# Performance work log

Hardware: AMD Instinct MI355X
Metric: run time of the kernel (lower is better)

Reference implementation:

```python
import jax, jax.numpy as jnp
import numpy as np

B, N, NB, E, H, A, K, D = 32, 512, 10, 1024, 256, 82, 4, 3


def setup_inputs() -> dict:
    key = jax.random.key(0)
    ks = iter(jax.random.split(key, 64))
    f = lambda shape: jax.random.normal(next(ks), shape, jnp.float32) * 0.05
    inp = {
        "atom_fea": jax.random.normal(next(ks), (B, N, A), jnp.float32),
        "bond_fea": jax.random.normal(next(ks), (B, E, 6), jnp.float32),
        "d_anb": jax.random.randint(next(ks), (B, N, NB), 0, N),
        "d_bnb": jax.random.randint(next(ks), (B, N, NB), 0, E),
        "d_nbs_mask": (jax.random.uniform(next(ks), (B, N, NB)) < 0.8).astype(jnp.float32),
        "d_mask": (jax.random.uniform(next(ks), (B, N)) < 0.9).astype(jnp.float32),
        "Wv": f((A, H)), "bv": f((H,)),
        "Wa_main": f((D, K, H, H)), "ba_main": f((D, K, H)),
        "Wa_super": f((D, K, H, H)), "ba_super": f((D, K, H)),
        "Wm": f((D, K, H, H)), "bm": f((D, K, H)),
        "Wbmm": f((D, K, H)), "bbmm": f((D, K)),
        "Wm2s": f((D, K * H, H)), "bm2s": f((D, H)),
        "Ws2m": f((D, H, H)), "bs2m": f((D, H)),
        "Wsup": f((D, H, H)), "bsup": f((D, H)),
        "Wzm1": f((D, H, H)), "bzm1": f((D, H)),
        "Wzm2": f((D, H, H)), "bzm2": f((D, H)),
        "Wzs1": f((D, H, H)), "bzs1": f((D, H)),
        "Wzs2": f((D, H, H)), "bzs2": f((D, H)),
        "Wu2": f((D, H + 6, H)), "bu2": f((D, H)),
        "Wu1": f((D, 2 * H, H)), "bu1": f((D, H)),
    }
    return inp


def mask_softmax(a, mask):
    a_max = jnp.max(a, -1, keepdims=True)
    e = jnp.exp(a - a_max) * mask
    return e / (jnp.sum(e, -1, keepdims=True) + 1e-6)


def _forward(atom_fea, bond_fea, d_nbs_mask, d_mask,
             Wv, bv, Wa_main, ba_main, Wa_super, ba_super, Wm, bm, Wbmm, bbmm,
             Wm2s, bm2s, Ws2m, bs2m, Wsup, bsup,
             Wzm1, bzm1, Wzm2, bzm2, Wzs1, bzs1, Wzs2, bzs2,
             Wu2, bu2, Wu1, bu1, d_anb, d_bnb):
    Bn = atom_fea.shape[0]
    bidx = jnp.arange(Bn)[:, None, None]
    # vertex embedding (default leaky_relu slope 0.01)
    vf = jax.nn.leaky_relu(atom_fea @ Wv + bv, 0.01)            # [B,N,H]
    sf = jnp.sum(vf * d_mask[:, :, None], axis=1, keepdims=True)  # [B,1,H]
    mask3 = d_nbs_mask[..., None]                               # [B,N,NB,1]
    for d in range(D):
        # --- multi-head main->super attention (vectorized over heads k) ---
        a_main = jnp.tanh(jnp.einsum('bnh,khj->bknj', vf, Wa_main[d]) + ba_main[d][None, :, None, :])
        a_super = jnp.tanh(jnp.einsum('boh,khj->bkoj', sf, Wa_super[d]) + ba_super[d][None, :, None, :])
        a = jnp.einsum('bknh,kh->bkn', a_main * a_super, Wbmm[d]) + bbmm[d][None, :, None]
        attn = mask_softmax(a, d_mask[:, None, :])               # [B,K,N]
        mvf = jnp.einsum('bnh,khj->bknj', vf, Wm[d]) + bm[d][None, :, None, :]
        m2s = jnp.einsum('bkn,bknh->bkh', attn, mvf).reshape(Bn, 1, K * H)
        main_to_super = jnp.tanh(m2s @ Wm2s[d] + bm2s[d])        # [B,1,H]
        # --- wln unit: gather neighbors, MLP, masked sum (slope 0.1) ---
        vnei = vf[bidx, d_anb]                                   # [B,N,NB,H]
        enei = bond_fea[bidx, d_bnb]                             # [B,N,NB,6]
        lnei = jnp.concatenate([vnei, enei], -1)                 # [B,N,NB,H+6]
        nei = jax.nn.leaky_relu(lnei @ Wu2[d] + bu2[d], 0.1)
        nei = jnp.sum(nei * mask3, axis=2)                       # [B,N,H]
        main_self = jax.nn.leaky_relu(jnp.concatenate([vf, nei], -1) @ Wu1[d] + bu1[d], 0.1)
        # --- GRU-style gated updates ---
        super_to_main = jnp.tanh(sf @ Ws2m[d] + bs2m[d])         # [B,1,H]
        super_self = jnp.tanh(sf @ Wsup[d] + bsup[d])            # [B,1,H]
        z_main = jax.nn.sigmoid(main_self @ Wzm1[d] + bzm1[d] + super_to_main @ Wzm2[d] + bzm2[d])
        vf = (1 - z_main) * main_self + z_main * super_to_main
        z_sup = jax.nn.sigmoid(super_self @ Wzs1[d] + bzs1[d] + main_to_super @ Wzs2[d] + bzs2[d])
        sf = (1 - z_sup) * super_self + z_sup * main_to_super    # [B,1,H]; sum over dim 1 is a no-op
    return vf, sf


def reference(atom_fea, bond_fea, d_anb, d_bnb, d_nbs_mask, d_mask,
              Wv, bv, Wa_main, ba_main, Wa_super, ba_super, Wm, bm, Wbmm, bbmm,
              Wm2s, bm2s, Ws2m, bs2m, Wsup, bsup,
              Wzm1, bzm1, Wzm2, bzm2, Wzs1, bzs1, Wzs2, bzs2,
              Wu2, bu2, Wu1, bu1):
    return _forward(atom_fea, bond_fea, d_nbs_mask, d_mask,
                    Wv, bv, Wa_main, ba_main, Wa_super, ba_super, Wm, bm, Wbmm, bbmm,
                    Wm2s, bm2s, Ws2m, bs2m, Wsup, bsup,
                    Wzm1, bzm1, Wzm2, bzm2, Wzs1, bzs1, Wzs2, bzs2,
                    Wu2, bu2, Wu1, bu1, d_anb, d_bnb)
```

## Files before the change

kernel.cpp:

```cpp
#include <hip/hip_runtime.h>
#include <hip/hip_bf16.h>

#define B_ 32
#define N_ 512
#define NB_ 10
#define E_ 1024
#define H_ 256
#define A_ 82
#define K_ 4
#define D_ 3
#define M_ (B_*N_)

typedef unsigned short u16;
typedef __attribute__((ext_vector_type(8))) short bf16x8;
typedef __attribute__((ext_vector_type(4))) float f32x4;

__device__ __forceinline__ float b2f(u16 u){
    unsigned int x = ((unsigned int)u) << 16;
    return __builtin_bit_cast(float, x);
}
__device__ __forceinline__ u16 f2b(float f){
    unsigned int x = __builtin_bit_cast(unsigned int, f);
    unsigned int lsb = (x >> 16) & 1u;
    x += 0x7fffu + lsb;
    return (u16)(x >> 16);
}
__device__ __forceinline__ float sigmoidf_(float x){ return 1.f/(1.f+expf(-x)); }

static constexpr int CVT_N[31] = {
    B_*E_*6, B_*N_*NB_, B_*N_,
    A_*H_, H_,
    D_*K_*H_*H_, D_*K_*H_, D_*K_*H_*H_, D_*K_*H_,
    D_*K_*H_*H_, D_*K_*H_, D_*K_*H_, D_*K_,
    D_*K_*H_*H_, D_*H_, D_*H_*H_, D_*H_,
    D_*H_*H_, D_*H_, D_*H_*H_, D_*H_,
    D_*H_*H_, D_*H_, D_*H_*H_, D_*H_,
    D_*H_*H_, D_*H_, D_*(H_+6)*H_, D_*H_,
    D_*2*H_*H_, D_*H_
};
struct Offs { long v[32]; };
static constexpr Offs mk_offs(){
    Offs o{}; o.v[0]=0;
    for(int i=0;i<31;i++) o.v[i+1]=o.v[i]+CVT_N[i];
    return o;
}
static constexpr Offs CVT_OFF = mk_offs();

struct Ptrs { const void* p[31]; };

__global__ void k_detect(const unsigned short* __restrict__ wv_raw, int* __restrict__ flag){
    float v = b2f(wv_raw[threadIdx.x]);
    bool plaus = (v==v) && (fabsf(v) < 100.0f);
    unsigned long long m = __ballot(plaus);
    if (threadIdx.x==0) *flag = (m == ~0ULL) ? 1 : 0;
}

__global__ void k_cvt(Ptrs ptrs, float* __restrict__ dst, const int* __restrict__ flag){
    int t = blockIdx.y;
    int n = CVT_N[t];
    int i4 = blockIdx.x*256 + threadIdx.x;
    if (i4*4 >= n) return;
    const void* src = ptrs.p[t];
    float4 o;
    if (*flag){
        ushort4 u = ((const ushort4*)src)[i4];
        o.x=b2f(u.x); o.y=b2f(u.y); o.z=b2f(u.z); o.w=b2f(u.w);
    } else {
        o = ((const float4*)src)[i4];
    }
    *(float4*)(dst + CVT_OFF.v[t] + (size_t)i4*4) = o;
}

__global__ void k_wt(const float* __restrict__ Wam, const float* __restrict__ Wu2,
                     const float* __restrict__ Wu1, const float* __restrict__ Wzm1,
                     u16* __restrict__ WT){
    int mi = blockIdx.z;
    const float* src;
    if (mi<12)      src = Wam  + (size_t)mi*H_*H_;
    else if (mi<15) src = Wu2  + (size_t)(mi-12)*(H_+6)*H_;
    else if (mi<18) src = Wu1  + (size_t)(mi-15)*2*H_*H_;
    else if (mi<21) src = Wu1  + (size_t)(mi-18)*2*H_*H_ + (size_t)H_*H_;
    else            src = Wzm1 + (size_t)(mi-21)*H_*H_;
    __shared__ float t[32][33];
    int x = threadIdx.x, y = threadIdx.y;
    int k0 = blockIdx.y*32, n0 = blockIdx.x*32;
    for(int yy=y; yy<32; yy+=8) t[yy][x] = src[(size_t)(k0+yy)*H_ + n0+x];
    __syncthreads();
    u16* dst = WT + ((size_t)mi*8 + (k0>>5))*(256*32);
    for(int yy=y; yy<32; yy+=8) dst[(size_t)(n0+yy)*32 + x] = f2b(t[x][yy]);
}

__global__ void k_embed(const u16* __restrict__ atom, const float* __restrict__ Wv,
                        const float* __restrict__ bv, float* __restrict__ vf,
                        const int* __restrict__ flag){
    __shared__ float arow[8][A_];
    int r0 = blockIdx.x*8; int j = threadIdx.x;
    int fl = *flag;
    for(int i=j;i<8*A_;i+=256){
        int r=i/A_, a=i-r*A_;
        arow[r][a] = fl ? b2f(atom[(size_t)(r0+r)*A_+a])
                        : ((const float*)atom)[(size_t)(r0+r)*A_+a];
    }
    __syncthreads();
    float acc[8];
    float bj = bv[j];
    #pragma unroll
    for(int r=0;r<8;r++) acc[r]=bj;
    for(int a=0;a<A_;a++){
        float w = Wv[a*H_+j];
        #pragma unroll
        for(int r=0;r<8;r++) acc[r] += arow[r][a]*w;
    }
    #pragma unroll
    for(int r=0;r<8;r++){
        float v = acc[r];
        vf[(size_t)(r0+r)*H_+j] = v>0.f ? v : 0.01f*v;
    }
}

__global__ void k_sf0(const float* __restrict__ vf, const float* __restrict__ dmask,
                      float* __restrict__ sf){
    int b = blockIdx.x, h = threadIdx.x;
    __shared__ float mk[N_];
    for(int n=threadIdx.x;n<N_;n+=256) mk[n] = dmask[b*N_+n];
    __syncthreads();
    float s=0.f;
    #pragma unroll 8
    for(int n=0;n<N_;n++) s += mk[n]*vf[((size_t)b*N_+n)*H_ + h];
    sf[b*H_+h]=s;
}

__global__ void k_s1(int d, const float* __restrict__ sf,
    const float* __restrict__ Was, const float* __restrict__ bas,
    const float* __restrict__ Wbmm,
    const float* __restrict__ Ws2m, const float* __restrict__ bs2m,
    const float* __restrict__ Wsup, const float* __restrict__ bsup,
    float* __restrict__ asw, float* __restrict__ s2m, float* __restrict__ ssf)
{
    int b = blockIdx.x, m = blockIdx.y, j = threadIdx.x;
    __shared__ float sfl[H_];
    sfl[j] = sf[b*H_+j];
    __syncthreads();
    const float* W; float bias;
    if (m < 4){ W = Was + (size_t)(d*K_+m)*H_*H_; bias = bas[(d*K_+m)*H_+j]; }
    else if (m==4){ W = Ws2m + (size_t)d*H_*H_; bias = bs2m[d*H_+j]; }
    else { W = Wsup + (size_t)d*H_*H_; bias = bsup[d*H_+j]; }
    float acc = bias;
    #pragma unroll 8
    for(int h=0;h<H_;h++) acc += sfl[h]*W[h*H_+j];
    float v = tanhf(acc);
    if (m < 4) asw[(b*K_+m)*H_+j] = v * Wbmm[(d*K_+m)*H_+j];
    else if (m==4) s2m[b*H_+j] = v;
    else ssf[b*H_+j] = v;
}

__global__ void k_s2(int d, const float* __restrict__ s2m,
    const float* __restrict__ Wzm2, const float* __restrict__ bzm2,
    float* __restrict__ stm2p)
{
    int b=blockIdx.x, c=blockIdx.y, j=threadIdx.x;
    __shared__ float xl[64];
    if (j<64) xl[j] = s2m[b*H_ + c*64 + j];
    __syncthreads();
    const float* W = Wzm2 + (size_t)d*H_*H_ + (size_t)(c*64)*H_;
    float acc = (c==0) ? bzm2[d*H_+j] : 0.f;
    #pragma unroll 8
    for(int h=0;h<64;h++) acc += xl[h]*W[h*H_+j];
    stm2p[((size_t)c*B_+b)*H_+j] = acc;
}

__device__ __forceinline__ void mfma_core_wt(const float* __restrict__ A,
    const u16* __restrict__ WTg, f32x4 acc[2][8],
    u16* __restrict__ Als, u16* __restrict__ Ws)
{
    const int LSA = 40, LSW = 40;
    int tid = threadIdx.x;
    int lane = tid & 63, wave = tid >> 6;
    int wy = wave >> 1, wx = wave & 1;
    int quad = lane >> 4, l15 = lane & 15;
    #pragma unroll
    for(int mt=0;mt<2;mt++)
        #pragma unroll
        for(int nt=0;nt<8;nt++) acc[mt][nt] = (f32x4){0.f,0.f,0.f,0.f};
    int arow = tid >> 2;
    int ak8  = (tid & 3) * 8;
    for(int k0=0;k0<H_;k0+=32){
        float4 a0 = *(const float4*)(A + (size_t)arow*H_ + k0 + ak8);
        float4 a1 = *(const float4*)(A + (size_t)arow*H_ + k0 + ak8 + 4);
        union { u16 u[8]; bf16x8 v; } ua;
        ua.u[0]=f2b(a0.x); ua.u[1]=f2b(a0.y); ua.u[2]=f2b(a0.z); ua.u[3]=f2b(a0.w);
        ua.u[4]=f2b(a1.x); ua.u[5]=f2b(a1.y); ua.u[6]=f2b(a1.z); ua.u[7]=f2b(a1.w);
        *(bf16x8*)(Als + arow*LSA + ak8) = ua.v;
        const u16* wsrc = WTg + (size_t)(k0>>5)*(256*32) + tid*32;
        #pragma unroll
        for(int c=0;c<4;c++)
            *(bf16x8*)(Ws + tid*LSW + c*8) = *(const bf16x8*)(wsrc + c*8);
        __syncthreads();
        bf16x8 af[2], bfr[8];
        #pragma unroll
        for(int mt=0;mt<2;mt++)
            af[mt] = *(const bf16x8*)(Als + (wy*32+mt*16+l15)*LSA + quad*8);
        #pragma unroll
        for(int nt=0;nt<8;nt++)
            bfr[nt] = *(const bf16x8*)(Ws + (wx*128+nt*16+l15)*LSW + quad*8);
        #pragma unroll
        for(int mt=0;mt<2;mt++)
            #pragma unroll
            for(int nt=0;nt<8;nt++)
                acc[mt][nt] = __builtin_amdgcn_mfma_f32_16x16x32_bf16(
                    af[mt], bfr[nt], acc[mt][nt], 0,0,0);
        __syncthreads();
    }
}

__global__ __launch_bounds__(256) void k_gemm_big(int d, const float* __restrict__ vf,
    const u16* __restrict__ WT, const float* __restrict__ ba_main,
    const float* __restrict__ bbmm, const float* __restrict__ bu1,
    const float* __restrict__ asw, float* __restrict__ score,
    float* __restrict__ proj_u2, float* __restrict__ pu1a)
{
    __shared__ u16 Als[64*40];
    __shared__ u16 Ws[256*40];
    __shared__ float sred[64][33];
    int m0 = blockIdx.x*64;
    int seg = blockIdx.y;
    int b = m0 >> 9;
    int mi;
    if (seg < 4)      mi = d*4+seg;
    else if (seg==4)  mi = 12+d;
    else              mi = 15+d;
    f32x4 acc[2][8];
    mfma_core_wt(vf + (size_t)m0*H_, WT + (size_t)mi*H_*H_, acc, Als, Ws);
    int tid=threadIdx.x, lane=tid&63, wave=tid>>6;
    int wy=wave>>1, wx=wave&1, quad=lane>>4, l15=lane&15;
    if (seg < 4){
        const float* aswp = asw + (size_t)(b*K_+seg)*H_;
        const float* bap  = ba_main + (size_t)(d*K_+seg)*H_;
        float bbv[8], awv[8];
        #pragma unroll
        for(int nt=0;nt<8;nt++){
            int col = wx*128+nt*16+l15;
            bbv[nt]=bap[col]; awv[nt]=aswp[col];
        }
        #pragma unroll
        for(int mt=0;mt<2;mt++)
            #pragma unroll
            for(int r=0;r<4;r++){
                float p=0.f;
                #pragma unroll
                for(int nt=0;nt<8;nt++)
                    p += tanhf(acc[mt][nt][r]+bbv[nt])*awv[nt];
                int row = wy*32+mt*16+quad*4+r;
                sred[row][wx*16+l15] = p;
            }
        __syncthreads();
        if (tid < 64){
            float s=0.f;
            #pragma unroll 8
            for(int i=0;i<32;i++) s += sred[tid][i];
            score[(size_t)(b*K_+seg)*N_ + (m0&511) + tid] = s + bbmm[d*K_+seg];
        }
    } else if (seg==4){
        #pragma unroll
        for(int mt=0;mt<2;mt++)
            #pragma unroll
            for(int nt=0;nt<8;nt++){
                int col = wx*128+nt*16+l15;
                #pragma unroll
                for(int r=0;r<4;r++){
                    int row = m0 + wy*32+mt*16+quad*4+r;
                    proj_u2[(size_t)row*H_+col] = acc[mt][nt][r];
                }
            }
    } else {
        const float* bp = bu1 + d*H_;
        #pragma unroll
        for(int mt=0;mt<2;mt++)
            #pragma unroll
            for(int nt=0;nt<8;nt++){
                int col = wx*128+nt*16+l15;
                float bb = bp[col];
                #pragma unroll
                for(int r=0;r<4;r++){
                    int row = m0 + wy*32+mt*16+quad*4+r;
                    pu1a[(size_t)row*H_+col] = acc[mt][nt][r] + bb;
                }
            }
    }
}

__global__ __launch_bounds__(256) void k_mainself(int d, const float* __restrict__ nei,
    const u16* __restrict__ WT, float* __restrict__ pu)
{
    __shared__ u16 Als[64*40];
    __shared__ u16 Ws[256*40];
    int m0 = blockIdx.x*64;
    f32x4 acc[2][8];
    mfma_core_wt(nei + (size_t)m0*H_, WT + (size_t)(18+d)*H_*H_, acc, Als, Ws);
    int tid=threadIdx.x, lane=tid&63, wave=tid>>6;
    int wy=wave>>1, wx=wave&1, quad=lane>>4, l15=lane&15;
    #pragma unroll
    for(int mt=0;mt<2;mt++)
        #pragma unroll
        for(int nt=0;nt<8;nt++){
            int col = wx*128+nt*16+l15;
            #pragma unroll
            for(int r=0;r<4;r++){
                int row = m0 + wy*32+mt*16+quad*4+r;
                float v = acc[mt][nt][r] + pu[(size_t)row*H_+col];
                v = v>0.f? v : 0.1f*v;
                pu[(size_t)row*H_+col] = v;
            }
        }
}

__global__ __launch_bounds__(256) void k_update(int d, const float* __restrict__ main_self,
    const u16* __restrict__ WT, const float* __restrict__ bzm1,
    const float* __restrict__ stm2p, const float* __restrict__ s2m, float* __restrict__ vf)
{
    __shared__ u16 Als[64*40];
    __shared__ u16 Ws[256*40];
    int m0 = blockIdx.x*64; int b = m0>>9;
    f32x4 acc[2][8];
    mfma_core_wt(main_self + (size_t)m0*H_, WT + (size_t)(21+d)*H_*H_, acc, Als, Ws);
    int tid=threadIdx.x, lane=tid&63, wave=tid>>6;
    int wy=wave>>1, wx=wave&1, quad=lane>>4, l15=lane&15;
    #pragma unroll
    for(int mt=0;mt<2;mt++)
        #pragma unroll
        for(int nt=0;nt<8;nt++){
            int col = wx*128+nt*16+l15;
            float bz = bzm1[d*H_+col];
            float st = stm2p[(size_t)(0*B_+b)*H_+col] + stm2p[(size_t)(1*B_+b)*H_+col]
                     + stm2p[(size_t)(2*B_+b)*H_+col] + stm2p[(size_t)(3*B_+b)*H_+col];
            float sm = s2m[b*H_+col];
            #pragma unroll
            for(int r=0;r<4;r++){
                int row = m0 + wy*32+mt*16+quad*4+r;
                float z = sigmoidf_(acc[mt][nt][r] + bz + st);
                float ms = main_self[(size_t)row*H_+col];
                vf[(size_t)row*H_+col] = (1.f-z)*ms + z*sm;
            }
        }
}

__global__ void k_softmax(float* __restrict__ score, const float* __restrict__ dmask,
                          float* __restrict__ sumattn){
    int b = blockIdx.x, k = blockIdx.y;
    int tid = threadIdx.x;
    __shared__ float sh[256];
    float* a = score + (size_t)(b*K_+k)*N_;
    float v0 = a[tid], v1 = a[tid+256];
    sh[tid]=fmaxf(v0,v1); __syncthreads();
    for(int s=128;s>0;s>>=1){ if(tid<s) sh[tid]=fmaxf(sh[tid],sh[tid+s]); __syncthreads(); }
    float m = sh[0]; __syncthreads();
    float e0 = expf(v0-m)*dmask[b*N_+tid], e1 = expf(v1-m)*dmask[b*N_+tid+256];
    sh[tid]=e0+e1; __syncthreads();
    for(int s=128;s>0;s>>=1){ if(tid<s) sh[tid]+=sh[tid+s]; __syncthreads(); }
    float S = sh[0];
    float inv = 1.f/(S+1e-6f);
    a[tid]=e0*inv; a[tid+256]=e1*inv;
    if(tid==0) sumattn[b*K_+k]=S*inv;
}

__global__ void k_t2(const float* __restrict__ attn, const float* __restrict__ vf,
                     float* __restrict__ tpart){
    int b=blockIdx.x, k=blockIdx.y, c=blockIdx.z, h=threadIdx.x;
    __shared__ float at[256];
    at[h] = attn[(size_t)(b*K_+k)*N_ + c*256 + h];
    __syncthreads();
    float acc=0.f;
    const float* vfp = vf + ((size_t)b*N_ + c*256)*H_ + h;
    #pragma unroll 8
    for(int n=0;n<256;n++) acc += at[n]*vfp[(size_t)n*H_];
    tpart[((size_t)(c*B_+b)*K_+k)*H_+h]=acc;
}

__global__ void k_m1(int d, const float* __restrict__ tpart, const float* __restrict__ sumattn,
    const float* __restrict__ Wm, const float* __restrict__ bm, float* __restrict__ m2s)
{
    int b=blockIdx.x, k=blockIdx.y, j=threadIdx.x;
    __shared__ float tl[H_];
    tl[j] = tpart[((size_t)(0*B_+b)*K_+k)*H_+j] + tpart[((size_t)(1*B_+b)*K_+k)*H_+j];
    __syncthreads();
    const float* W = Wm + (size_t)(d*K_+k)*H_*H_;
    float acc = sumattn[b*K_+k]*bm[(d*K_+k)*H_+j];
    #pragma unroll 8
    for(int h=0;h<H_;h++) acc += tl[h]*W[h*H_+j];
    m2s[(size_t)(b*K_+k)*H_+j]=acc;
}

__global__ void k_m2(int d, const float* __restrict__ m2s, const float* __restrict__ Wm2s,
                     float* __restrict__ mtsp)
{
    int b=blockIdx.x, c=blockIdx.y, j=threadIdx.x;
    __shared__ float xl[H_];
    xl[j]=m2s[(size_t)(b*K_+c)*H_+j];
    __syncthreads();
    const float* W = Wm2s + (size_t)d*(K_*H_)*H_ + (size_t)(c*H_)*H_;
    float acc=0.f;
    #pragma unroll 8
    for(int h=0;h<H_;h++) acc += xl[h]*W[h*H_+j];
    mtsp[((size_t)c*B_+b)*H_+j]=acc;
}

__global__ void k_mts(int d, const float* __restrict__ mtsp, const float* __restrict__ bm2s,
                      float* __restrict__ mts){
    int b=blockIdx.x, j=threadIdx.x;
    float acc = bm2s[d*H_+j];
    #pragma unroll
    for(int c=0;c<4;c++) acc += mtsp[((size_t)c*B_+b)*H_+j];
    mts[b*H_+j]=tanhf(acc);
}

__global__ void k_m3(int d, const float* __restrict__ ssf, const float* __restrict__ mts,
    const float* __restrict__ Wzs1, const float* __restrict__ Wzs2,
    float* __restrict__ p1, float* __restrict__ p2)
{
    int b=blockIdx.x, m=blockIdx.y, j=threadIdx.x;
    __shared__ float xl[H_];
    const float* x = m ? mts : ssf;
    xl[j]=x[b*H_+j];
    __syncthreads();
    const float* W = (m ? Wzs2 : Wzs1) + (size_t)d*H_*H_;
    float acc=0.f;
    #pragma unroll 8
    for(int h=0;h<H_;h++) acc += xl[h]*W[h*H_+j];
    (m ? p2 : p1)[b*H_+j]=acc;
}

__global__ void k_sfup(int d, const float* __restrict__ p1, const float* __restrict__ p2,
    const float* __restrict__ bzs1, const float* __restrict__ bzs2,
    const float* __restrict__ ssf, const float* __restrict__ mts, float* __restrict__ sf)
{
    int b=blockIdx.x, j=threadIdx.x;
    float z = sigmoidf_(p1[b*H_+j]+bzs1[d*H_+j]+p2[b*H_+j]+bzs2[d*H_+j]);
    sf[b*H_+j]=(1.f-z)*ssf[b*H_+j]+z*mts[b*H_+j];
}

__global__ void k_nei(int d, const int* __restrict__ anb, const int* __restrict__ bnb,
    const float* __restrict__ nbm, const float* __restrict__ bond,
    const float* __restrict__ Wu2, const float* __restrict__ bu2,
    const float* __restrict__ proj_u2, float* __restrict__ nei)
{
    __shared__ float W2s[6][256];
    __shared__ float bfeat[NB_][6];
    __shared__ int ai[NB_]; __shared__ int bi[NB_]; __shared__ float mk[NB_];
    int row = blockIdx.x; int b = row >> 9; int h = threadIdx.x;
    const float* W2 = Wu2 + (size_t)d*(H_+6)*H_ + (size_t)H_*H_;
    for(int i=h;i<6*H_;i+=256) W2s[i>>8][i&255] = W2[i];
    if (h<NB_){ ai[h]=anb[row*NB_+h]; bi[h]=bnb[row*NB_+h]; mk[h]=nbm[row*NB_+h]; }
    __syncthreads();
    if (h<NB_*6){ int jn=h/6, i=h-jn*6; bfeat[jn][i]=bond[((size_t)b*E_+bi[jn])*6+i]; }
    __syncthreads();
    float bu = bu2[d*H_+h];
    float acc=0.f;
    #pragma unroll
    for(int jn=0;jn<NB_;jn++){
        float v = proj_u2[((size_t)b*N_+ai[jn])*H_+h] + bu;
        #pragma unroll
        for(int i=0;i<6;i++) v += bfeat[jn][i]*W2s[i][h];
        v = v>0.f? v : 0.1f*v;
        acc += mk[jn]*v;
    }
    nei[(size_t)row*H_+h]=acc;
}

__global__ void k_out(const float* __restrict__ vf, const float* __restrict__ sf,
                      void* __restrict__ out, const int* __restrict__ flag){
    int idx = blockIdx.x*256 + threadIdx.x;
    const int total = M_*H_ + B_*H_;
    if (idx >= total) return;
    float v = (idx < M_*H_) ? vf[idx] : sf[idx - M_*H_];
    if (*flag) ((unsigned short*)out)[idx] = f2b(v);
    else       ((float*)out)[idx] = v;
}

extern "C" void kernel_launch(void* const* d_in, const int* in_sizes, int n_in,
                              void* d_out, int out_size, void* d_ws, size_t ws_size,
                              hipStream_t stream)
{
    const int* anb = (const int*)d_in[2];
    const int* bnb = (const int*)d_in[3];

    float* ws   = (float*)d_ws;
    int*   flag = (int*)ws;
    float* cvt  = ws + 64;
    float* p    = cvt + ((CVT_OFF.v[31] + 63) & ~63L);
    float* vf        = p; p += (size_t)M_*H_;
    float* proj_u2   = p; p += (size_t)M_*H_;
    float* proj_u1a  = p; p += (size_t)M_*H_;
    float* nei       = p; p += (size_t)M_*H_;
    float* sf        = p; p += B_*H_;
    float* score     = p; p += B_*K_*N_;
    float* sumattn   = p; p += B_*K_;
    float* asw       = p; p += B_*K_*H_;
    float* s2m       = p; p += B_*H_;
    float* ssf       = p; p += B_*H_;
    float* stm2p     = p; p += 4*B_*H_;
    float* tpart     = p; p += 2*B_*K_*H_;
    float* m2s       = p; p += B_*K_*H_;
    float* mtsp      = p; p += 4*B_*H_;
    float* mts       = p; p += B_*H_;
    float* p1        = p; p += B_*H_;
    float* p2        = p; p += B_*H_;
    u16*   WT        = (u16*)p;

    const float* cBond = cvt + CVT_OFF.v[0];
    const float* cNbm  = cvt + CVT_OFF.v[1];
    const float* cDm   = cvt + CVT_OFF.v[2];
    const float* cWv   = cvt + CVT_OFF.v[3];
    const float* cbv   = cvt + CVT_OFF.v[4];
    const float* cWam  = cvt + CVT_OFF.v[5];
    const float* cbam  = cvt + CVT_OFF.v[6];
    const float* cWas  = cvt + CVT_OFF.v[7];
    const float* cbas  = cvt + CVT_OFF.v[8];
    const float* cWm   = cvt + CVT_OFF.v[9];
    const float* cbm   = cvt + CVT_OFF.v[10];
    const float* cWbmm = cvt + CVT_OFF.v[11];
    const float* cbbmm = cvt + CVT_OFF.v[12];
    const float* cWm2s = cvt + CVT_OFF.v[13];
    const float* cbm2s = cvt + CVT_OFF.v[14];
    const float* cWs2m = cvt + CVT_OFF.v[15];
    const float* cbs2m = cvt + CVT_OFF.v[16];
    const float* cWsup = cvt + CVT_OFF.v[17];
    const float* cbsup = cvt + CVT_OFF.v[18];
    const float* cWzm1 = cvt + CVT_OFF.v[19];
    const float* cbzm1 = cvt + CVT_OFF.v[20];
    const float* cWzm2 = cvt + CVT_OFF.v[21];
    const float* cbzm2 = cvt + CVT_OFF.v[22];
    const float* cWzs1 = cvt + CVT_OFF.v[23];
    const float* cbzs1 = cvt + CVT_OFF.v[24];
    const float* cWzs2 = cvt + CVT_OFF.v[25];
    const float* cbzs2 = cvt + CVT_OFF.v[26];
    const float* cWu2  = cvt + CVT_OFF.v[27];
    const float* cbu2  = cvt + CVT_OFF.v[28];
    const float* cWu1  = cvt + CVT_OFF.v[29];
    const float* cbu1  = cvt + CVT_OFF.v[30];

    Ptrs ptrs;
    {
        int idx[31] = {1,4,5,6,7,8,9,10,11,12,13,14,15,16,17,18,19,20,21,
                       22,23,24,25,26,27,28,29,30,31,32,33};
        for(int i=0;i<31;i++) ptrs.p[i] = d_in[idx[i]];
    }

    k_detect<<<1,64,0,stream>>>((const unsigned short*)d_in[6], flag);
    {
        int maxv4 = (D_*K_*H_*H_ + 3)/4;
        int gx = (maxv4 + 255)/256;
        k_cvt<<<dim3(gx,31),256,0,stream>>>(ptrs, cvt, flag);
    }
    k_wt<<<dim3(8,8,24),dim3(32,8),0,stream>>>(cWam, cWu2, cWu1, cWzm1, WT);

    k_embed<<<M_/8,256,0,stream>>>((const u16*)d_in[0], cWv, cbv, vf, flag);
    k_sf0<<<B_,256,0,stream>>>(vf, cDm, sf);
    for(int d=0; d<D_; d++){
        k_s1<<<dim3(B_,6),256,0,stream>>>(d, sf, cWas, cbas, cWbmm,
                                          cWs2m, cbs2m, cWsup, cbsup, asw, s2m, ssf);
        k_s2<<<dim3(B_,4),256,0,stream>>>(d, s2m, cWzm2, cbzm2, stm2p);
        k_gemm_big<<<dim3(M_/64,6),256,0,stream>>>(d, vf, WT, cbam, cbbmm, cbu1,
                                                   asw, score, proj_u2, proj_u1a);
        k_softmax<<<dim3(B_,K_),256,0,stream>>>(score, cDm, sumattn);
        k_t2<<<dim3(B_,K_,2),256,0,stream>>>(score, vf, tpart);
        k_m1<<<dim3(B_,K_),256,0,stream>>>(d, tpart, sumattn, cWm, cbm, m2s);
        k_m2<<<dim3(B_,4),256,0,stream>>>(d, m2s, cWm2s, mtsp);
        k_mts<<<B_,256,0,stream>>>(d, mtsp, cbm2s, mts);
        k_m3<<<dim3(B_,2),256,0,stream>>>(d, ssf, mts, cWzs1, cWzs2, p1, p2);
        k_sfup<<<B_,256,0,stream>>>(d, p1, p2, cbzs1, cbzs2, ssf, mts, sf);
        k_nei<<<M_,256,0,stream>>>(d, anb, bnb, cNbm, cBond, cWu2, cbu2, proj_u2, nei);
        k_mainself<<<M_/64,256,0,stream>>>(d, nei, WT, proj_u1a);
        k_update<<<M_/64,256,0,stream>>>(d, proj_u1a, WT, cbzm1, stm2p, s2m, vf);
    }
    k_out<<<(M_*H_+B_*H_+255)/256,256,0,stream>>>(vf, sf, d_out, flag);
}
```

Measured before the change: 746.0 us.

## Store per-node activation buffers in bf16 instead of fp32

Converts the large per-atom intermediate buffers (vertex features, projected u2, neighbour aggregate, main_self) from fp32 to bf16 storage across all producer and consumer kernels. GEMM A-operand loads now copy bf16 directly into LDS with no per-tile conversion. This roughly halves memory traffic for the bandwidth-bound gather, reduction and GEMM-input kernels. In exchange, intermediate values are rounded to bf16 between stages, which adds numerical error across the depth iterations.

```diff
diff --git a/kernel.cpp b/kernel.cpp
--- a/kernel.cpp
+++ b/kernel.cpp
@@ -91,7 +91,7 @@
 }
 
 __global__ void k_embed(const u16* __restrict__ atom, const float* __restrict__ Wv,
-                        const float* __restrict__ bv, float* __restrict__ vf,
+                        const float* __restrict__ bv, u16* __restrict__ vfb,
                         const int* __restrict__ flag){
     __shared__ float arow[8][A_];
     int r0 = blockIdx.x*8; int j = threadIdx.x;
@@ -114,11 +114,11 @@
     #pragma unroll
     for(int r=0;r<8;r++){
         float v = acc[r];
-        vf[(size_t)(r0+r)*H_+j] = v>0.f ? v : 0.01f*v;
-    }
-}
-
-__global__ void k_sf0(const float* __restrict__ vf, const float* __restrict__ dmask,
+        vfb[(size_t)(r0+r)*H_+j] = f2b(v>0.f ? v : 0.01f*v);
+    }
+}
+
+__global__ void k_sf0(const u16* __restrict__ vfb, const float* __restrict__ dmask,
                       float* __restrict__ sf){
     int b = blockIdx.x, h = threadIdx.x;
     __shared__ float mk[N_];
@@ -126,7 +126,7 @@
     __syncthreads();
     float s=0.f;
     #pragma unroll 8
-    for(int n=0;n<N_;n++) s += mk[n]*vf[((size_t)b*N_+n)*H_ + h];
+    for(int n=0;n<N_;n++) s += mk[n]*b2f(vfb[((size_t)b*N_+n)*H_ + h]);
     sf[b*H_+h]=s;
 }
 
@@ -169,7 +169,7 @@
     stm2p[((size_t)c*B_+b)*H_+j] = acc;
 }
 
-__device__ __forceinline__ void mfma_core_wt(const float* __restrict__ A,
+__device__ __forceinline__ void mfma_core_bt(const u16* __restrict__ A,
     const u16* __restrict__ WTg, f32x4 acc[2][8],
     u16* __restrict__ Als, u16* __restrict__ Ws)
 {
@@ -185,12 +185,8 @@
     int arow = tid >> 2;
     int ak8  = (tid & 3) * 8;
     for(int k0=0;k0<H_;k0+=32){
-        float4 a0 = *(const float4*)(A + (size_t)arow*H_ + k0 + ak8);
-        float4 a1 = *(const float4*)(A + (size_t)arow*H_ + k0 + ak8 + 4);
-        union { u16 u[8]; bf16x8 v; } ua;
-        ua.u[0]=f2b(a0.x); ua.u[1]=f2b(a0.y); ua.u[2]=f2b(a0.z); ua.u[3]=f2b(a0.w);
-        ua.u[4]=f2b(a1.x); ua.u[5]=f2b(a1.y); ua.u[6]=f2b(a1.z); ua.u[7]=f2b(a1.w);
-        *(bf16x8*)(Als + arow*LSA + ak8) = ua.v;
+        *(bf16x8*)(Als + arow*LSA + ak8) =
+            *(const bf16x8*)(A + (size_t)arow*H_ + k0 + ak8);
         const u16* wsrc = WTg + (size_t)(k0>>5)*(256*32) + tid*32;
         #pragma unroll
         for(int c=0;c<4;c++)
@@ -213,11 +209,11 @@
     }
 }
 
-__global__ __launch_bounds__(256) void k_gemm_big(int d, const float* __restrict__ vf,
+__global__ __launch_bounds__(256) void k_gemm_big(int d, const u16* __restrict__ vfb,
     const u16* __restrict__ WT, const float* __restrict__ ba_main,
     const float* __restrict__ bbmm, const float* __restrict__ bu1,
     const float* __restrict__ asw, float* __restrict__ score,
-    float* __restrict__ proj_u2, float* __restrict__ pu1a)
+    u16* __restrict__ projb, float* __restrict__ pu1a)
 {
     __shared__ u16 Als[64*40];
     __shared__ u16 Ws[256*40];
@@ -230,7 +226,7 @@
     else if (seg==4)  mi = 12+d;
     else              mi = 15+d;
     f32x4 acc[2][8];
-    mfma_core_wt(vf + (size_t)m0*H_, WT + (size_t)mi*H_*H_, acc, Als, Ws);
+    mfma_core_bt(vfb + (size_t)m0*H_, WT + (size_t)mi*H_*H_, acc, Als, Ws);
     int tid=threadIdx.x, lane=tid&63, wave=tid>>6;
     int wy=wave>>1, wx=wave&1, quad=lane>>4, l15=lane&15;
     if (seg < 4){
@@ -269,7 +265,7 @@
                 #pragma unroll
                 for(int r=0;r<4;r++){
                     int row = m0 + wy*32+mt*16+quad*4+r;
-                    proj_u2[(size_t)row*H_+col] = acc[mt][nt][r];
+                    projb[(size_t)row*H_+col] = f2b(acc[mt][nt][r]);
                 }
             }
     } else {
@@ -289,14 +285,14 @@
     }
 }
 
-__global__ __launch_bounds__(256) void k_mainself(int d, const float* __restrict__ nei,
-    const u16* __restrict__ WT, float* __restrict__ pu)
+__global__ __launch_bounds__(256) void k_mainself(int d, const u16* __restrict__ neib,
+    const u16* __restrict__ WT, const float* __restrict__ pu1a, u16* __restrict__ msb)
 {
     __shared__ u16 Als[64*40];
     __shared__ u16 Ws[256*40];
     int m0 = blockIdx.x*64;
     f32x4 acc[2][8];
-    mfma_core_wt(nei + (size_t)m0*H_, WT + (size_t)(18+d)*H_*H_, acc, Als, Ws);
+    mfma_core_bt(neib + (size_t)m0*H_, WT + (size_t)(18+d)*H_*H_, acc, Als, Ws);
     int tid=threadIdx.x, lane=tid&63, wave=tid>>6;
     int wy=wave>>1, wx=wave&1, quad=lane>>4, l15=lane&15;
     #pragma unroll
@@ -307,22 +303,22 @@
             #pragma unroll
             for(int r=0;r<4;r++){
                 int row = m0 + wy*32+mt*16+quad*4+r;
-                float v = acc[mt][nt][r] + pu[(size_t)row*H_+col];
+                float v = acc[mt][nt][r] + pu1a[(size_t)row*H_+col];
                 v = v>0.f? v : 0.1f*v;
-                pu[(size_t)row*H_+col] = v;
+                msb[(size_t)row*H_+col] = f2b(v);
             }
         }
 }
 
-__global__ __launch_bounds__(256) void k_update(int d, const float* __restrict__ main_self,
+__global__ __launch_bounds__(256) void k_update(int d, const u16* __restrict__ msb,
     const u16* __restrict__ WT, const float* __restrict__ bzm1,
-    const float* __restrict__ stm2p, const float* __restrict__ s2m, float* __restrict__ vf)
+    const float* __restrict__ stm2p, const float* __restrict__ s2m, u16* __restrict__ vfb)
 {
     __shared__ u16 Als[64*40];
     __shared__ u16 Ws[256*40];
     int m0 = blockIdx.x*64; int b = m0>>9;
     f32x4 acc[2][8];
-    mfma_core_wt(main_self + (size_t)m0*H_, WT + (size_t)(21+d)*H_*H_, acc, Als, Ws);
+    mfma_core_bt(msb + (size_t)m0*H_, WT + (size_t)(21+d)*H_*H_, acc, Als, Ws);
     int tid=threadIdx.x, lane=tid&63, wave=tid>>6;
     int wy=wave>>1, wx=wave&1, quad=lane>>4, l15=lane&15;
     #pragma unroll
@@ -338,8 +334,8 @@
             for(int r=0;r<4;r++){
                 int row = m0 + wy*32+mt*16+quad*4+r;
                 float z = sigmoidf_(acc[mt][nt][r] + bz + st);
-                float ms = main_self[(size_t)row*H_+col];
-                vf[(size_t)row*H_+col] = (1.f-z)*ms + z*sm;
+                float ms = b2f(msb[(size_t)row*H_+col]);
+                vfb[(size_t)row*H_+col] = f2b((1.f-z)*ms + z*sm);
             }
         }
 }
@@ -363,16 +359,16 @@
     if(tid==0) sumattn[b*K_+k]=S*inv;
 }
 
-__global__ void k_t2(const float* __restrict__ attn, const float* __restrict__ vf,
+__global__ void k_t2(const float* __restrict__ attn, const u16* __restrict__ vfb,
                      float* __restrict__ tpart){
     int b=blockIdx.x, k=blockIdx.y, c=blockIdx.z, h=threadIdx.x;
     __shared__ float at[256];
     at[h] = attn[(size_t)(b*K_+k)*N_ + c*256 + h];
     __syncthreads();
     float acc=0.f;
-    const float* vfp = vf + ((size_t)b*N_ + c*256)*H_ + h;
-    #pragma unroll 8
-    for(int n=0;n<256;n++) acc += at[n]*vfp[(size_t)n*H_];
+    const u16* vfp = vfb + ((size_t)b*N_ + c*256)*H_ + h;
+    #pragma unroll 8
+    for(int n=0;n<256;n++) acc += at[n]*b2f(vfp[(size_t)n*H_]);
     tpart[((size_t)(c*B_+b)*K_+k)*H_+h]=acc;
 }
 
@@ -441,7 +437,7 @@
 __global__ void k_nei(int d, const int* __restrict__ anb, const int* __restrict__ bnb,
     const float* __restrict__ nbm, const float* __restrict__ bond,
     const float* __restrict__ Wu2, const float* __restrict__ bu2,
-    const float* __restrict__ proj_u2, float* __restrict__ nei)
+    const u16* __restrict__ projb, u16* __restrict__ neib)
 {
     __shared__ float W2s[6][256];
     __shared__ float bfeat[NB_][6];
@@ -457,23 +453,25 @@
     float acc=0.f;
     #pragma unroll
     for(int jn=0;jn<NB_;jn++){
-        float v = proj_u2[((size_t)b*N_+ai[jn])*H_+h] + bu;
+        float v = b2f(projb[((size_t)b*N_+ai[jn])*H_+h]) + bu;
         #pragma unroll
         for(int i=0;i<6;i++) v += bfeat[jn][i]*W2s[i][h];
         v = v>0.f? v : 0.1f*v;
         acc += mk[jn]*v;
     }
-    nei[(size_t)row*H_+h]=acc;
-}
-
-__global__ void k_out(const float* __restrict__ vf, const float* __restrict__ sf,
+    neib[(size_t)row*H_+h]=f2b(acc);
+}
+
+__global__ void k_out(const u16* __restrict__ vfb, const float* __restrict__ sf,
                       void* __restrict__ out, const int* __restrict__ flag){
     int idx = blockIdx.x*256 + threadIdx.x;
     const int total = M_*H_ + B_*H_;
     if (idx >= total) return;
-    float v = (idx < M_*H_) ? vf[idx] : sf[idx - M_*H_];
-    if (*flag) ((unsigned short*)out)[idx] = f2b(v);
-    else       ((float*)out)[idx] = v;
+    if (*flag){
+        ((u16*)out)[idx] = (idx < M_*H_) ? vfb[idx] : f2b(sf[idx - M_*H_]);
+    } else {
+        ((float*)out)[idx] = (idx < M_*H_) ? b2f(vfb[idx]) : sf[idx - M_*H_];
+    }
 }
 
 extern "C" void kernel_launch(void* const* d_in, const int* in_sizes, int n_in,
@@ -487,13 +485,10 @@
     int*   flag = (int*)ws;
     float* cvt  = ws + 64;
     float* p    = cvt + ((CVT_OFF.v[31] + 63) & ~63L);
-    float* vf        = p; p += (size_t)M_*H_;
-    float* proj_u2   = p; p += (size_t)M_*H_;
-    float* proj_u1a  = p; p += (size_t)M_*H_;
-    float* nei       = p; p += (size_t)M_*H_;
+    float* pu1a      = p; p += (size_t)M_*H_;
     float* sf        = p; p += B_*H_;
     float* score     = p; p += B_*K_*N_;
-    float* sumattn   = p; p += B_*K_;
+    float* sumattn   = p; p += 128;
     float* asw       = p; p += B_*K_*H_;
     float* s2m       = p; p += B_*H_;
     float* ssf       = p; p += B_*H_;
@@ -505,6 +500,10 @@
     float* p1        = p; p += B_*H_;
     float* p2        = p; p += B_*H_;
     u16*   WT        = (u16*)p;
+    u16*   vfb       = WT  + (size_t)24*H_*H_;
+    u16*   projb     = vfb + (size_t)M_*H_;
+    u16*   neib     = projb + (size_t)M_*H_;
+    u16*   msb      = neib  + (size_t)M_*H_;
 
     const float* cBond = cvt + CVT_OFF.v[0];
     const float* cNbm  = cvt + CVT_OFF.v[1];
@@ -553,24 +552,24 @@
     }
     k_wt<<<dim3(8,8,24),dim3(32,8),0,stream>>>(cWam, cWu2, cWu1, cWzm1, WT);
 
-    k_embed<<<M_/8,256,0,stream>>>((const u16*)d_in[0], cWv, cbv, vf, flag);
-    k_sf0<<<B_,256,0,stream>>>(vf, cDm, sf);
+    k_embed<<<M_/8,256,0,stream>>>((const u16*)d_in[0], cWv, cbv, vfb, flag);
+    k_sf0<<<B_,256,0,stream>>>(vfb, cDm, sf);
     for(int d=0; d<D_; d++){
         k_s1<<<dim3(B_,6),256,0,stream>>>(d, sf, cWas, cbas, cWbmm,
                                           cWs2m, cbs2m, cWsup, cbsup, asw, s2m, ssf);
         k_s2<<<dim3(B_,4),256,0,stream>>>(d, s2m, cWzm2, cbzm2, stm2p);
-        k_gemm_big<<<dim3(M_/64,6),256,0,stream>>>(d, vf, WT, cbam, cbbmm, cbu1,
-                                                   asw, score, proj_u2, proj_u1a);
+        k_gemm_big<<<dim3(M_/64,6),256,0,stream>>>(d, vfb, WT, cbam, cbbmm, cbu1,
+                                                   asw, score, projb, pu1a);
         k_softmax<<<dim3(B_,K_),256,0,stream>>>(score, cDm, sumattn);
-        k_t2<<<dim3(B_,K_,2),256,0,stream>>>(score, vf, tpart);
+        k_t2<<<dim3(B_,K_,2),256,0,stream>>>(score, vfb, tpart);
         k_m1<<<dim3(B_,K_),256,0,stream>>>(d, tpart, sumattn, cWm, cbm, m2s);
         k_m2<<<dim3(B_,4),256,0,stream>>>(d, m2s, cWm2s, mtsp);
         k_mts<<<B_,256,0,stream>>>(d, mtsp, cbm2s, mts);
         k_m3<<<dim3(B_,2),256,0,stream>>>(d, ssf, mts, cWzs1, cWzs2, p1, p2);
         k_sfup<<<B_,256,0,stream>>>(d, p1, p2, cbzs1, cbzs2, ssf, mts, sf);
-        k_nei<<<M_,256,0,stream>>>(d, anb, bnb, cNbm, cBond, cWu2, cbu2, proj_u2, nei);
-        k_mainself<<<M_/64,256,0,stream>>>(d, nei, WT, proj_u1a);
-        k_update<<<M_/64,256,0,stream>>>(d, proj_u1a, WT, cbzm1, stm2p, s2m, vf);
-    }
-    k_out<<<(M_*H_+B_*H_+255)/256,256,0,stream>>>(vf, sf, d_out, flag);
-}
+        k_nei<<<M_,256,0,stream>>>(d, anb, bnb, cNbm, cBond, cWu2, cbu2, projb, neib);
+        k_mainself<<<M_/64,256,0,stream>>>(d, neib, WT, pu1a, msb);
+        k_update<<<M_/64,256,0,stream>>>(d, msb, WT, cbzm1, stm2p, s2m, vfb);
+    }
+    k_out<<<(M_*H_+B_*H_+255)/256,256,0,stream>>>(vfb, sf, d_out, flag);
+}
```

After: 804.5 us. +7.8%, slower.
